# Kernel optimization log

Measured on AMD Instinct MI355X. Metric: run time of the kernel, lower is better.

The kernel has to match this reference:

```python
import jax, jax.numpy as jnp
import numpy as np

DN = ('NCDHW', 'OIDHW', 'NCDHW')

def conv3d(x, w, b):
    y = jax.lax.conv_general_dilated(x, w, window_strides=(1, 1, 1),
                                     padding=[(1, 1)] * 3, dimension_numbers=DN)
    return y + b[None, :, None, None, None]

def setup_inputs() -> dict:
    key = jax.random.key(0)
    ks = jax.random.split(key, 9)
    B, Cin, D, H, W = 2, 64, 8, 16, 16
    s = 0.05
    return {
        'x': jax.random.normal(ks[0], (B, Cin, D, H, W), jnp.float32),
        'w_key': jax.random.normal(ks[1], (32, Cin, 3, 3, 3), jnp.float32) * s,
        'b_key': jax.random.normal(ks[2], (32,), jnp.float32) * s,
        'w_query': jax.random.normal(ks[3], (32, Cin, 3, 3, 3), jnp.float32) * s,
        'b_query': jax.random.normal(ks[4], (32,), jnp.float32) * s,
        'w_value': jax.random.normal(ks[5], (32, Cin, 3, 3, 3), jnp.float32) * s,
        'b_value': jax.random.normal(ks[6], (32,), jnp.float32) * s,
        'w_alter': jax.random.normal(ks[7], (64, 32, 3, 3, 3), jnp.float32) * s,
        'b_alter': jax.random.normal(ks[8], (64,), jnp.float32) * s,
    }

def reference(x, w_key, b_key, w_query, b_query, w_value, b_value, w_alter, b_alter):
    k = conv3d(x, w_key, b_key)      # [B,32,D,H,W]
    q = conv3d(x, w_query, b_query)
    v = conv3d(x, w_value, b_value)
    B, C, D, H, W = k.shape
    N = D * H * W
    kf = k.reshape(B, C, N)
    qf = q.reshape(B, C, N)
    vf = v.reshape(B, C, N)
    qp = jnp.transpose(qf, (1, 2, 0))  # [C,N,B]
    kp = jnp.transpose(kf, (1, 0, 2))  # [C,B,N]
    vp = jnp.transpose(vf, (1, 2, 0))  # [C,N,B]
    # attn: [C,N,N]; torch softmax over dim=1 (the query/row N axis)
    attn = jax.nn.softmax(jnp.einsum('cnb,cbm->cnm', qp, kp), axis=1)
    out = jnp.einsum('cnm,cmb->cnb', attn, vp)  # [C,N,B]
    # torch .view reinterprets the contiguous [C,N,B] buffer as [B,C,D,H,W]
    out = out.reshape(B, C, D, H, W)
    out = conv3d(out, w_alter, b_alter)  # [B,64,D,H,W]
    return x + out
```

## Files before the change

kernel.cpp:

```cpp
#include <hip/hip_runtime.h>

#define BB 2
#define CIN 64
#define CQ 32
#define DD 8
#define HH 16
#define WWW 16
#define NN 2048
#define NHW 256
#define COUT 64

#define XPLANE 324
#define CI_OUT 8

#define NPART 8
#define LOG2E 1.44269504088896340736f

__device__ __forceinline__ float fast_exp2(float x) {
#if __has_builtin(__builtin_amdgcn_exp2f)
    return __builtin_amdgcn_exp2f(x);
#else
    return exp2f(x);
#endif
}

__global__ __launch_bounds__(256) void init_kernel(
    const float* __restrict__ bk, const float* __restrict__ bq, const float* __restrict__ bv,
    const float* __restrict__ ba, const float* __restrict__ x,
    float* __restrict__ kout, float* __restrict__ qout, float* __restrict__ vout,
    float* __restrict__ out)
{
    int i = blockIdx.x * 256 + threadIdx.x;
    if (i < BB * CQ * NN) {
        int co = (i >> 11) & 31;
        kout[i] = bk[co];
        qout[i] = bq[co];
        vout[i] = bv[co];
    } else {
        int j = i - BB * CQ * NN;
        int co = (j >> 11) & 63;
        out[j] = x[j] + ba[co];
    }
}

__global__ __launch_bounds__(256, 4) void conv_qkv_kernel(
    const float* __restrict__ x,
    const float* __restrict__ wk, const float* __restrict__ wq, const float* __restrict__ wv,
    float* __restrict__ kout, float* __restrict__ qout, float* __restrict__ vout)
{
    int bid   = blockIdx.x;
    int split = bid & 7;
    int co2   = (bid >> 3) & 15;
    int dp    = (bid >> 7) & 3;
    int b     = bid >> 9;
    int co0   = co2 << 1;
    int ci0   = split << 3;
    int d0    = dp << 1;

    __shared__ float xl[4 * 4 * XPLANE];
    __shared__ float wlds[6 * 8 * 27];

    int tid = threadIdx.x;
    int h  = tid >> 4;
    int w  = tid & 15;
    int wr = (h + 1) * 18 + (w + 1);
    int rb = h * 18 + w;

    {
        const float* ws0 = wk + ((size_t)(co0    ) * CIN + ci0) * 27;
        const float* ws1 = wk + ((size_t)(co0 + 1) * CIN + ci0) * 27;
        const float* ws2 = wq + ((size_t)(co0    ) * CIN + ci0) * 27;
        const float* ws3 = wq + ((size_t)(co0 + 1) * CIN + ci0) * 27;
        const float* ws4 = wv + ((size_t)(co0    ) * CIN + ci0) * 27;
        const float* ws5 = wv + ((size_t)(co0 + 1) * CIN + ci0) * 27;
        if (tid < 216) {
            wlds[0 * 216 + tid] = ws0[tid];
            wlds[1 * 216 + tid] = ws1[tid];
            wlds[2 * 216 + tid] = ws2[tid];
            wlds[3 * 216 + tid] = ws3[tid];
            wlds[4 * 216 + tid] = ws4[tid];
            wlds[5 * 216 + tid] = ws5[tid];
        }
    }

    const float* xb = x + ((size_t)b * CIN + ci0) * NN;

    float r[16];
    #pragma unroll
    for (int p = 0; p < 4; ++p) {
        int dd = d0 - 1 + p;
        bool ok = (dd >= 0) && (dd < DD);
        #pragma unroll
        for (int cc = 0; cc < 4; ++cc)
            r[cc * 4 + p] = ok ? xb[(size_t)cc * NN + dd * NHW + tid] : 0.f;
    }
    for (int i = tid; i < 16 * XPLANE; i += 256) xl[i] = 0.f;
    __syncthreads();
    #pragma unroll
    for (int j = 0; j < 16; ++j)
        xl[j * XPLANE + wr] = r[j];

    float s0a = 0.f, s0b = 0.f, s1a = 0.f, s1b = 0.f, s2a = 0.f, s2b = 0.f;
    float s3a = 0.f, s3b = 0.f, s4a = 0.f, s4b = 0.f, s5a = 0.f, s5b = 0.f;

    #pragma unroll 1
    for (int it = 0; it < 8; it += 4) {
        __syncthreads();
        if (it + 4 < 8) {
            #pragma unroll
            for (int p = 0; p < 4; ++p) {
                int dd = d0 - 1 + p;
                bool ok = (dd >= 0) && (dd < DD);
                #pragma unroll
                for (int cc = 0; cc < 4; ++cc)
                    r[cc * 4 + p] = ok ? xb[(size_t)(it + 4 + cc) * NN + dd * NHW + tid] : 0.f;
            }
        }

        for (int cc = 0; cc < 4; ++cc) {
            int cil = it + cc;
            const float* wl0 = wlds + (0 * 8 + cil) * 27;
            const float* wl1 = wlds + (1 * 8 + cil) * 27;
            const float* wl2 = wlds + (2 * 8 + cil) * 27;
            const float* wl3 = wlds + (3 * 8 + cil) * 27;
            const float* wl4 = wlds + (4 * 8 + cil) * 27;
            const float* wl5 = wlds + (5 * 8 + cil) * 27;
            const float* xp  = xl + cc * 4 * XPLANE + rb;
            #pragma unroll
            for (int kh = 0; kh < 3; ++kh) {
                #pragma unroll
                for (int kw = 0; kw < 3; ++kw) {
                    int o = kh * 18 + kw;
                    float x0 = xp[o];
                    float x1 = xp[XPLANE + o];
                    float x2 = xp[2 * XPLANE + o];
                    float x3 = xp[3 * XPLANE + o];
                    #define TAP(KD, XA, XB) { \
                        int t = KD * 9 + kh * 3 + kw; \
                        float w0v = wl0[t], w1v = wl1[t], w2v = wl2[t]; \
                        float w3v = wl3[t], w4v = wl4[t], w5v = wl5[t]; \
                        s0a = fmaf(XA, w0v, s0a); s0b = fmaf(XB, w0v, s0b); \
                        s1a = fmaf(XA, w1v, s1a); s1b = fmaf(XB, w1v, s1b); \
                        s2a = fmaf(XA, w2v, s2a); s2b = fmaf(XB, w2v, s2b); \
                        s3a = fmaf(XA, w3v, s3a); s3b = fmaf(XB, w3v, s3b); \
                        s4a = fmaf(XA, w4v, s4a); s4b = fmaf(XB, w4v, s4b); \
                        s5a = fmaf(XA, w5v, s5a); s5b = fmaf(XB, w5v, s5b); }
                    TAP(0, x0, x1)
                    TAP(1, x1, x2)
                    TAP(2, x2, x3)
                    #undef TAP
                }
            }
        }

        __syncthreads();
        if (it + 4 < 8) {
            #pragma unroll
            for (int j = 0; j < 16; ++j)
                xl[j * XPLANE + wr] = r[j];
        }
    }

    size_t oA = ((size_t)b * CQ + co0) * NN + d0 * NHW + tid;
    unsafeAtomicAdd(&kout[oA],            s0a);
    unsafeAtomicAdd(&kout[oA + NHW],      s0b);
    unsafeAtomicAdd(&kout[oA + NN],       s1a);
    unsafeAtomicAdd(&kout[oA + NN + NHW], s1b);
    unsafeAtomicAdd(&qout[oA],            s2a);
    unsafeAtomicAdd(&qout[oA + NHW],      s2b);
    unsafeAtomicAdd(&qout[oA + NN],       s3a);
    unsafeAtomicAdd(&qout[oA + NN + NHW], s3b);
    unsafeAtomicAdd(&vout[oA],            s4a);
    unsafeAtomicAdd(&vout[oA + NHW],      s4b);
    unsafeAtomicAdd(&vout[oA + NN],       s5a);
    unsafeAtomicAdd(&vout[oA + NN + NHW], s5b);
}

__global__ __launch_bounds__(256) void mz_partial_kernel(
    const float* __restrict__ kbuf, const float* __restrict__ qbuf,
    float* __restrict__ pmax, float* __restrict__ psum)
{
    int bid = blockIdx.x;
    int nchunk = bid & 7;
    int mtile  = (bid >> 3) & 3;
    int c      = bid >> 5;

    __shared__ float q0l[256], q1l[256];
    int tid = threadIdx.x;
    int n0 = nchunk * 256;
    if (tid < 64) {
        float4 v = ((const float4*)(qbuf + (size_t)c * NN + n0))[tid];
        v.x *= LOG2E; v.y *= LOG2E; v.z *= LOG2E; v.w *= LOG2E;
        ((float4*)q0l)[tid] = v;
    } else if (tid < 128) {
        float4 v = ((const float4*)(qbuf + (size_t)(CQ + c) * NN + n0))[tid - 64];
        v.x *= LOG2E; v.y *= LOG2E; v.z *= LOG2E; v.w *= LOG2E;
        ((float4*)q1l)[tid - 64] = v;
    }
    __syncthreads();

    int m = mtile * 512 + tid * 2;
    float2 k0 = *(const float2*)(kbuf + (size_t)c * NN + m);
    float2 k1 = *(const float2*)(kbuf + (size_t)(CQ + c) * NN + m);

    const float4* q0v = (const float4*)q0l;
    const float4* q1v = (const float4*)q1l;

    float mxa = -1e30f, mxb = -1e30f;
    #pragma unroll 4
    for (int i = 0; i < 64; ++i) {
        float4 a = q0v[i], b4 = q1v[i];
        float sa0 = fmaf(k0.x, a.x, k1.x * b4.x);
        float sa1 = fmaf(k0.x, a.y, k1.x * b4.y);
        float sa2 = fmaf(k0.x, a.z, k1.x * b4.z);
        float sa3 = fmaf(k0.x, a.w, k1.x * b4.w);
        mxa = fmaxf(mxa, fmaxf(fmaxf(sa0, sa1), fmaxf(sa2, sa3)));
        float sb0 = fmaf(k0.y, a.x, k1.y * b4.x);
        float sb1 = fmaf(k0.y, a.y, k1.y * b4.y);
        float sb2 = fmaf(k0.y, a.z, k1.y * b4.z);
        float sb3 = fmaf(k0.y, a.w, k1.y * b4.w);
        mxb = fmaxf(mxb, fmaxf(fmaxf(sb0, sb1), fmaxf(sb2, sb3)));
    }

    float nma = -mxa, nmb = -mxb;
    float za = 0.f, zb = 0.f;
    #pragma unroll 4
    for (int i = 0; i < 64; ++i) {
        float4 a = q0v[i], b4 = q1v[i];
        za += fast_exp2(fmaf(k0.x, a.x, fmaf(k1.x, b4.x, nma)))
            + fast_exp2(fmaf(k0.x, a.y, fmaf(k1.x, b4.y, nma)))
            + fast_exp2(fmaf(k0.x, a.z, fmaf(k1.x, b4.z, nma)))
            + fast_exp2(fmaf(k0.x, a.w, fmaf(k1.x, b4.w, nma)));
        zb += fast_exp2(fmaf(k0.y, a.x, fmaf(k1.y, b4.x, nmb)))
            + fast_exp2(fmaf(k0.y, a.y, fmaf(k1.y, b4.y, nmb)))
            + fast_exp2(fmaf(k0.y, a.z, fmaf(k1.y, b4.z, nmb)))
            + fast_exp2(fmaf(k0.y, a.w, fmaf(k1.y, b4.w, nmb)));
    }
    size_t o = ((size_t)c * NPART + nchunk) * NN + m;
    float2 rm; rm.x = mxa; rm.y = mxb;
    float2 rz; rz.x = za;  rz.y = zb;
    *(float2*)(pmax + o) = rm;
    *(float2*)(psum + o) = rz;
}

__global__ __launch_bounds__(256) void att_partial_kernel(
    const float* __restrict__ kbuf, const float* __restrict__ qbuf,
    const float* __restrict__ vbuf,
    const float* __restrict__ pmax, const float* __restrict__ psum,
    float* __restrict__ parts)
{
    int bid = blockIdx.x;
    int mchunk = bid & 7;
    int ntile  = (bid >> 3) & 3;
    int c      = bid >> 5;

    __shared__ float k0l[256], k1l[256], vz0l[256], vz1l[256], nMl[256];
    int tid = threadIdx.x;
    {
        int m = mchunk * 256 + tid;
        float pj[NPART];
        float M = -1e30f;
        #pragma unroll
        for (int j = 0; j < NPART; ++j) {
            pj[j] = pmax[((size_t)c * NPART + j) * NN + m];
            M = fmaxf(M, pj[j]);
        }
        float z = 0.f;
        #pragma unroll
        for (int j = 0; j < NPART; ++j)
            z += psum[((size_t)c * NPART + j) * NN + m] * fast_exp2(pj[j] - M);
        float rz = 1.f / z;
        k0l[tid]  = kbuf[(size_t)c * NN + m];
        k1l[tid]  = kbuf[(size_t)(CQ + c) * NN + m];
        vz0l[tid] = vbuf[(size_t)c * NN + m] * rz;
        vz1l[tid] = vbuf[(size_t)(CQ + c) * NN + m] * rz;
        nMl[tid]  = -M;
    }
    __syncthreads();

    int n = ntile * 512 + tid * 2;
    float2 q0 = *(const float2*)(qbuf + (size_t)c * NN + n);
    float2 q1 = *(const float2*)(qbuf + (size_t)(CQ + c) * NN + n);
    q0.x *= LOG2E; q0.y *= LOG2E;
    q1.x *= LOG2E; q1.y *= LOG2E;

    const float4* k0v = (const float4*)k0l;
    const float4* k1v = (const float4*)k1l;
    const float4* v0v = (const float4*)vz0l;
    const float4* v1v = (const float4*)vz1l;
    const float4* nMv = (const float4*)nMl;

    float a00 = 0.f, a01 = 0.f;
    float a10 = 0.f, a11 = 0.f;

    #pragma unroll 2
    for (int i = 0; i < 64; ++i) {
        float4 kk0 = k0v[i], kk1 = k1v[i], w0 = v0v[i], w1 = v1v[i], nm = nMv[i];
        #define ATTS(KX,K1X,W0X,W1X,NMX) { \
            float e0 = fast_exp2(fmaf(q0.x, KX, fmaf(q1.x, K1X, NMX))); \
            float e1 = fast_exp2(fmaf(q0.y, KX, fmaf(q1.y, K1X, NMX))); \
            a00 = fmaf(e0, W0X, a00); a10 = fmaf(e0, W1X, a10); \
            a01 = fmaf(e1, W0X, a01); a11 = fmaf(e1, W1X, a11); }
        ATTS(kk0.x, kk1.x, w0.x, w1.x, nm.x)
        ATTS(kk0.y, kk1.y, w0.y, w1.y, nm.y)
        ATTS(kk0.z, kk1.z, w0.z, w1.z, nm.z)
        ATTS(kk0.w, kk1.w, w0.w, w1.w, nm.w)
        #undef ATTS
    }

    float* dst = parts + (size_t)mchunk * (CQ * NN * BB);
    size_t base = ((size_t)c * NN + n) * BB;
    float4 r0; r0.x = a00; r0.y = a10; r0.z = a01; r0.w = a11;
    *(float4*)(dst + base) = r0;
}

__global__ __launch_bounds__(256) void combine_kernel(
    const float* __restrict__ parts, float* __restrict__ ybuf)
{
    int i = blockIdx.x * 256 + threadIdx.x;
    float4 s = ((const float4*)parts)[i];
    #pragma unroll
    for (int j = 1; j < NPART; ++j) {
        float4 p = ((const float4*)(parts + (size_t)j * (CQ * NN * BB)))[i];
        s.x += p.x; s.y += p.y; s.z += p.z; s.w += p.w;
    }
    ((float4*)ybuf)[i] = s;
}

__global__ __launch_bounds__(256, 4) void conv_out_kernel(
    const float* __restrict__ ybuf,
    const float* __restrict__ wa,
    float* __restrict__ out)
{
    int bid   = blockIdx.x;
    int split = bid & 3;
    int cog   = (bid >> 2) & 15;
    int d     = (bid >> 6) & 7;
    int b     = bid >> 9;
    int co0   = cog << 2;
    int ci0   = split << 3;

    __shared__ float yl[CI_OUT * 3 * XPLANE];

    int tid = threadIdx.x;
    int h  = tid >> 4;
    int w  = tid & 15;
    int wr = (h + 1) * 18 + (w + 1);
    int rb = h * 18 + w;

    const float* yb = ybuf + ((size_t)b * CQ + ci0) * NN;

    float r[CI_OUT * 3];
    #pragma unroll
    for (int kd = 0; kd < 3; ++kd) {
        int dd = d + kd - 1;
        bool ok = (dd >= 0) && (dd < DD);
        #pragma unroll
        for (int cc = 0; cc < CI_OUT; ++cc)
            r[cc * 3 + kd] = ok ? yb[(size_t)cc * NN + dd * NHW + tid] : 0.f;
    }
    for (int i = tid; i < CI_OUT * 3 * XPLANE; i += 256) yl[i] = 0.f;
    __syncthreads();
    #pragma unroll
    for (int j = 0; j < CI_OUT * 3; ++j)
        yl[j * XPLANE + wr] = r[j];
    __syncthreads();

    float a0 = 0.f, a1 = 0.f, a2 = 0.f, a3 = 0.f;

    for (int cc = 0; cc < CI_OUT; ++cc) {
        int ci = ci0 + cc;
        const float* w0 = wa + ((size_t)(co0 + 0) * CQ + ci) * 27;
        const float* w1 = wa + ((size_t)(co0 + 1) * CQ + ci) * 27;
        const float* w2 = wa + ((size_t)(co0 + 2) * CQ + ci) * 27;
        const float* w3 = wa + ((size_t)(co0 + 3) * CQ + ci) * 27;
        const float* yp = yl + cc * 3 * XPLANE + rb;
        #pragma unroll
        for (int kd = 0; kd < 3; ++kd) {
            int dd = d + kd - 1;
            if (dd < 0 || dd >= DD) continue;
            #pragma unroll
            for (int kh = 0; kh < 3; ++kh) {
                #pragma unroll
                for (int kw = 0; kw < 3; ++kw) {
                    float yv = yp[kd * XPLANE + kh * 18 + kw];
                    int t = kd * 9 + kh * 3 + kw;
                    a0 = fmaf(yv, w0[t], a0);
                    a1 = fmaf(yv, w1[t], a1);
                    a2 = fmaf(yv, w2[t], a2);
                    a3 = fmaf(yv, w3[t], a3);
                }
            }
        }
    }

    size_t o = ((size_t)b * COUT + co0) * NN + d * NHW + tid;
    unsafeAtomicAdd(&out[o],          a0);
    unsafeAtomicAdd(&out[o + NN],     a1);
    unsafeAtomicAdd(&out[o + 2 * NN], a2);
    unsafeAtomicAdd(&out[o + 3 * NN], a3);
}

extern "C" void kernel_launch(void* const* d_in, const int* in_sizes, int n_in,
                              void* d_out, int out_size, void* d_ws, size_t ws_size,
                              hipStream_t stream) {
    const float* x  = (const float*)d_in[0];
    const float* wk = (const float*)d_in[1];
    const float* bk = (const float*)d_in[2];
    const float* wq = (const float*)d_in[3];
    const float* bq = (const float*)d_in[4];
    const float* wv = (const float*)d_in[5];
    const float* bv = (const float*)d_in[6];
    const float* wa = (const float*)d_in[7];
    const float* ba = (const float*)d_in[8];
    float* out = (float*)d_out;

    float* ws   = (float*)d_ws;
    float* kbuf = ws;
    float* qbuf = kbuf + BB * CQ * NN;
    float* vbuf = qbuf + BB * CQ * NN;
    float* pmax = vbuf + BB * CQ * NN;
    float* psum = pmax + CQ * NPART * NN;
    float* parts = psum + CQ * NPART * NN;
    float* ybuf = kbuf;

    init_kernel<<<1536, 256, 0, stream>>>(bk, bq, bv, ba, x, kbuf, qbuf, vbuf, out);
    conv_qkv_kernel<<<1024, 256, 0, stream>>>(x, wk, wq, wv, kbuf, qbuf, vbuf);
    mz_partial_kernel<<<1024, 256, 0, stream>>>(kbuf, qbuf, pmax, psum);
    att_partial_kernel<<<1024, 256, 0, stream>>>(kbuf, qbuf, vbuf, pmax, psum, parts);
    combine_kernel<<<128, 256, 0, stream>>>(parts, ybuf);
    conv_out_kernel<<<1024, 256, 0, stream>>>(ybuf, wa, out);
}
```

Measured before the change: 111.9 us.

## Retile QKV conv so each thread computes four adjacent W outputs over four depths

The QKV convolution now has each block cover four output depth slices instead of two, with each thread producing 4 consecutive W outputs, so the grid drops to 512 blocks. Input planes are padded to 20 columns so rows can be read with float4/float2 loads and reused across the kw taps, cutting LDS reads per FMA. Weights are no longer staged in LDS; they are read per-ci straight from global memory, relying on uniform cached loads. The cost is more registers (launch bounds relaxed to 2 blocks per CU), fewer blocks, and scalar weight loads on the critical path.

```diff
diff --git a/kernel.cpp b/kernel.cpp
--- a/kernel.cpp
+++ b/kernel.cpp
@@ -12,6 +12,11 @@
 
 #define XPLANE 324
 #define CI_OUT 8
+
+#define QROWS 18
+#define QCOLS 20
+#define QPLANE (QROWS * QCOLS)
+#define QCI 4
 
 #define NPART 8
 #define LOG2E 1.44269504088896340736f
@@ -43,7 +48,7 @@
     }
 }
 
-__global__ __launch_bounds__(256, 4) void conv_qkv_kernel(
+__global__ __launch_bounds__(256, 2) void conv_qkv_kernel(
     const float* __restrict__ x,
     const float* __restrict__ wk, const float* __restrict__ wq, const float* __restrict__ wv,
     float* __restrict__ kout, float* __restrict__ qout, float* __restrict__ vout)
@@ -51,129 +56,137 @@
     int bid   = blockIdx.x;
     int split = bid & 7;
     int co2   = (bid >> 3) & 15;
-    int dp    = (bid >> 7) & 3;
-    int b     = bid >> 9;
+    int dq    = (bid >> 7) & 1;
+    int b     = bid >> 8;
     int co0   = co2 << 1;
     int ci0   = split << 3;
-    int d0    = dp << 1;
-
-    __shared__ float xl[4 * 4 * XPLANE];
-    __shared__ float wlds[6 * 8 * 27];
+    int d0    = dq << 2;
+
+    __shared__ float xl[QCI * 6 * QPLANE];
 
     int tid = threadIdx.x;
-    int h  = tid >> 4;
-    int w  = tid & 15;
-    int wr = (h + 1) * 18 + (w + 1);
-    int rb = h * 18 + w;
-
-    {
-        const float* ws0 = wk + ((size_t)(co0    ) * CIN + ci0) * 27;
-        const float* ws1 = wk + ((size_t)(co0 + 1) * CIN + ci0) * 27;
-        const float* ws2 = wq + ((size_t)(co0    ) * CIN + ci0) * 27;
-        const float* ws3 = wq + ((size_t)(co0 + 1) * CIN + ci0) * 27;
-        const float* ws4 = wv + ((size_t)(co0    ) * CIN + ci0) * 27;
-        const float* ws5 = wv + ((size_t)(co0 + 1) * CIN + ci0) * 27;
-        if (tid < 216) {
-            wlds[0 * 216 + tid] = ws0[tid];
-            wlds[1 * 216 + tid] = ws1[tid];
-            wlds[2 * 216 + tid] = ws2[tid];
-            wlds[3 * 216 + tid] = ws3[tid];
-            wlds[4 * 216 + tid] = ws4[tid];
-            wlds[5 * 216 + tid] = ws5[tid];
-        }
-    }
+    int hw = tid >> 4;
+    int ww = tid & 15;
+    int wr = (hw + 1) * QCOLS + (ww + 1);
+    int pn  = tid >> 6;
+    int rem = tid & 63;
+    int h   = rem >> 2;
+    int wqi = rem & 3;
 
     const float* xb = x + ((size_t)b * CIN + ci0) * NN;
 
-    float r[16];
-    #pragma unroll
-    for (int p = 0; p < 4; ++p) {
+    float r[QCI * 6];
+    #pragma unroll
+    for (int p = 0; p < 6; ++p) {
         int dd = d0 - 1 + p;
-        bool ok = (dd >= 0) && (dd < DD);
+        if (dd >= 0 && dd < DD) {
+            #pragma unroll
+            for (int cl = 0; cl < QCI; ++cl)
+                r[cl * 6 + p] = xb[(size_t)cl * NN + dd * NHW + tid];
+        }
+    }
+    for (int i = tid; i < QCI * 6 * QPLANE; i += 256) xl[i] = 0.f;
+    __syncthreads();
+    #pragma unroll
+    for (int p = 0; p < 6; ++p) {
+        int dd = d0 - 1 + p;
+        if (dd >= 0 && dd < DD) {
+            #pragma unroll
+            for (int cl = 0; cl < QCI; ++cl)
+                xl[cl * 6 * QPLANE + p * QPLANE + wr] = r[cl * 6 + p];
+        }
+    }
+
+    float acc[6][4];
+    #pragma unroll
+    for (int s = 0; s < 6; ++s)
         #pragma unroll
-        for (int cc = 0; cc < 4; ++cc)
-            r[cc * 4 + p] = ok ? xb[(size_t)cc * NN + dd * NHW + tid] : 0.f;
-    }
-    for (int i = tid; i < 16 * XPLANE; i += 256) xl[i] = 0.f;
-    __syncthreads();
-    #pragma unroll
-    for (int j = 0; j < 16; ++j)
-        xl[j * XPLANE + wr] = r[j];
-
-    float s0a = 0.f, s0b = 0.f, s1a = 0.f, s1b = 0.f, s2a = 0.f, s2b = 0.f;
-    float s3a = 0.f, s3b = 0.f, s4a = 0.f, s4b = 0.f, s5a = 0.f, s5b = 0.f;
+        for (int o = 0; o < 4; ++o) acc[s][o] = 0.f;
 
     #pragma unroll 1
-    for (int it = 0; it < 8; it += 4) {
+    for (int ph = 0; ph < 2; ++ph) {
         __syncthreads();
-        if (it + 4 < 8) {
-            #pragma unroll
-            for (int p = 0; p < 4; ++p) {
+        if (ph == 0) {
+            #pragma unroll
+            for (int p = 0; p < 6; ++p) {
                 int dd = d0 - 1 + p;
-                bool ok = (dd >= 0) && (dd < DD);
-                #pragma unroll
-                for (int cc = 0; cc < 4; ++cc)
-                    r[cc * 4 + p] = ok ? xb[(size_t)(it + 4 + cc) * NN + dd * NHW + tid] : 0.f;
-            }
-        }
-
-        for (int cc = 0; cc < 4; ++cc) {
-            int cil = it + cc;
-            const float* wl0 = wlds + (0 * 8 + cil) * 27;
-            const float* wl1 = wlds + (1 * 8 + cil) * 27;
-            const float* wl2 = wlds + (2 * 8 + cil) * 27;
-            const float* wl3 = wlds + (3 * 8 + cil) * 27;
-            const float* wl4 = wlds + (4 * 8 + cil) * 27;
-            const float* wl5 = wlds + (5 * 8 + cil) * 27;
-            const float* xp  = xl + cc * 4 * XPLANE + rb;
-            #pragma unroll
-            for (int kh = 0; kh < 3; ++kh) {
-                #pragma unroll
-                for (int kw = 0; kw < 3; ++kw) {
-                    int o = kh * 18 + kw;
-                    float x0 = xp[o];
-                    float x1 = xp[XPLANE + o];
-                    float x2 = xp[2 * XPLANE + o];
-                    float x3 = xp[3 * XPLANE + o];
-                    #define TAP(KD, XA, XB) { \
-                        int t = KD * 9 + kh * 3 + kw; \
-                        float w0v = wl0[t], w1v = wl1[t], w2v = wl2[t]; \
-                        float w3v = wl3[t], w4v = wl4[t], w5v = wl5[t]; \
-                        s0a = fmaf(XA, w0v, s0a); s0b = fmaf(XB, w0v, s0b); \
-                        s1a = fmaf(XA, w1v, s1a); s1b = fmaf(XB, w1v, s1b); \
-                        s2a = fmaf(XA, w2v, s2a); s2b = fmaf(XB, w2v, s2b); \
-                        s3a = fmaf(XA, w3v, s3a); s3b = fmaf(XB, w3v, s3b); \
-                        s4a = fmaf(XA, w4v, s4a); s4b = fmaf(XB, w4v, s4b); \
-                        s5a = fmaf(XA, w5v, s5a); s5b = fmaf(XB, w5v, s5b); }
-                    TAP(0, x0, x1)
-                    TAP(1, x1, x2)
-                    TAP(2, x2, x3)
-                    #undef TAP
+                if (dd >= 0 && dd < DD) {
+                    #pragma unroll
+                    for (int cl = 0; cl < QCI; ++cl)
+                        r[cl * 6 + p] = xb[(size_t)(QCI + cl) * NN + dd * NHW + tid];
                 }
             }
         }
 
+        #pragma unroll 1
+        for (int cl = 0; cl < QCI; ++cl) {
+            int ci = ci0 + ph * QCI + cl;
+            const float* wk0 = wk + ((size_t)co0 * CIN + ci) * 27;
+            const float* wk1 = wk0 + (size_t)CIN * 27;
+            const float* wq0 = wq + ((size_t)co0 * CIN + ci) * 27;
+            const float* wq1 = wq0 + (size_t)CIN * 27;
+            const float* wv0 = wv + ((size_t)co0 * CIN + ci) * 27;
+            const float* wv1 = wv0 + (size_t)CIN * 27;
+            const float* xp  = xl + cl * 6 * QPLANE + pn * QPLANE + h * QCOLS + wqi * 4;
+
+            #pragma unroll
+            for (int kd = 0; kd < 3; ++kd) {
+                float ws[6][9];
+                #pragma unroll
+                for (int j = 0; j < 9; ++j) {
+                    int t = kd * 9 + j;
+                    ws[0][j] = wk0[t]; ws[1][j] = wk1[t];
+                    ws[2][j] = wq0[t]; ws[3][j] = wq1[t];
+                    ws[4][j] = wv0[t]; ws[5][j] = wv1[t];
+                }
+                #pragma unroll
+                for (int kh = 0; kh < 3; ++kh) {
+                    const float* xr = xp + kd * QPLANE + kh * QCOLS;
+                    float4 xa  = *(const float4*)xr;
+                    float2 xb2 = *(const float2*)(xr + 4);
+                    float xw[6] = {xa.x, xa.y, xa.z, xa.w, xb2.x, xb2.y};
+                    #pragma unroll
+                    for (int kw = 0; kw < 3; ++kw) {
+                        int t = kh * 3 + kw;
+                        #pragma unroll
+                        for (int o = 0; o < 4; ++o) {
+                            float xv = xw[o + kw];
+                            acc[0][o] = fmaf(ws[0][t], xv, acc[0][o]);
+                            acc[1][o] = fmaf(ws[1][t], xv, acc[1][o]);
+                            acc[2][o] = fmaf(ws[2][t], xv, acc[2][o]);
+                            acc[3][o] = fmaf(ws[3][t], xv, acc[3][o]);
+                            acc[4][o] = fmaf(ws[4][t], xv, acc[4][o]);
+                            acc[5][o] = fmaf(ws[5][t], xv, acc[5][o]);
+                        }
+                    }
+                }
+            }
+        }
+
         __syncthreads();
-        if (it + 4 < 8) {
-            #pragma unroll
-            for (int j = 0; j < 16; ++j)
-                xl[j * XPLANE + wr] = r[j];
-        }
-    }
-
-    size_t oA = ((size_t)b * CQ + co0) * NN + d0 * NHW + tid;
-    unsafeAtomicAdd(&kout[oA],            s0a);
-    unsafeAtomicAdd(&kout[oA + NHW],      s0b);
-    unsafeAtomicAdd(&kout[oA + NN],       s1a);
-    unsafeAtomicAdd(&kout[oA + NN + NHW], s1b);
-    unsafeAtomicAdd(&qout[oA],            s2a);
-    unsafeAtomicAdd(&qout[oA + NHW],      s2b);
-    unsafeAtomicAdd(&qout[oA + NN],       s3a);
-    unsafeAtomicAdd(&qout[oA + NN + NHW], s3b);
-    unsafeAtomicAdd(&vout[oA],            s4a);
-    unsafeAtomicAdd(&vout[oA + NHW],      s4b);
-    unsafeAtomicAdd(&vout[oA + NN],       s5a);
-    unsafeAtomicAdd(&vout[oA + NN + NHW], s5b);
+        if (ph == 0) {
+            #pragma unroll
+            for (int p = 0; p < 6; ++p) {
+                int dd = d0 - 1 + p;
+                if (dd >= 0 && dd < DD) {
+                    #pragma unroll
+                    for (int cl = 0; cl < QCI; ++cl)
+                        xl[cl * 6 * QPLANE + p * QPLANE + wr] = r[cl * 6 + p];
+                }
+            }
+        }
+    }
+
+    size_t o0 = ((size_t)b * CQ + co0) * NN + (d0 + pn) * NHW + h * WWW + wqi * 4;
+    #pragma unroll
+    for (int o = 0; o < 4; ++o) {
+        unsafeAtomicAdd(&kout[o0 + o],      acc[0][o]);
+        unsafeAtomicAdd(&kout[o0 + NN + o], acc[1][o]);
+        unsafeAtomicAdd(&qout[o0 + o],      acc[2][o]);
+        unsafeAtomicAdd(&qout[o0 + NN + o], acc[3][o]);
+        unsafeAtomicAdd(&vout[o0 + o],      acc[4][o]);
+        unsafeAtomicAdd(&vout[o0 + NN + o], acc[5][o]);
+    }
 }
 
 __global__ __launch_bounds__(256) void mz_partial_kernel(
@@ -425,7 +438,7 @@
     float* ybuf = kbuf;
 
     init_kernel<<<1536, 256, 0, stream>>>(bk, bq, bv, ba, x, kbuf, qbuf, vbuf, out);
-    conv_qkv_kernel<<<1024, 256, 0, stream>>>(x, wk, wq, wv, kbuf, qbuf, vbuf);
+    conv_qkv_kernel<<<512, 256, 0, stream>>>(x, wk, wq, wv, kbuf, qbuf, vbuf);
     mz_partial_kernel<<<1024, 256, 0, stream>>>(kbuf, qbuf, pmax, psum);
     att_partial_kernel<<<1024, 256, 0, stream>>>(kbuf, qbuf, vbuf, pmax, psum, parts);
     combine_kernel<<<128, 256, 0, stream>>>(parts, ybuf);
```

Result: slower. 126.7 us (+13.1%).
